# Performance work log

Hardware: AMD Instinct MI355X
Metric: run time of the kernel (lower is better)

The kernel has to match this reference:

```python
import jax, jax.numpy as jnp
import numpy as np
from jax import lax

# module config (matches init_kwargs)
IN_CHANNELS = 1
NUM_OR = 8               # 360 / angle_res(45)
THRESHOLD = 0.9
WINDOW = (5, 5)
STRIDE = (1, 1)
WINDOW_SCALE = float(WINDOW[0] * WINDOW[1])
NORMALIZE_COUNT = True   # normalize_count=True -> avg counts (avg_pool2d semantics)


def setup_inputs() -> dict:
    key = jax.random.key(0)
    k1, k2 = jax.random.split(key)
    x = jax.random.normal(k1, (16, IN_CHANNELS, 1024, 1024), dtype=jnp.float32)
    # edge-orientation masks (Sobel rotations in the original; values are fixed
    # buffers, so random stand-ins preserve the exact compute pattern)
    masks = jax.random.normal(k2, (IN_CHANNELS * NUM_OR, 1, 3, 3), dtype=jnp.float32)
    return {"x": x, "masks": masks}


def reference(x, masks):
    # grouped edge-filter conv: [B,C,H,W] x [C*O,1,3,3] -> [B,C*O,H-2,W-2]
    y = lax.conv_general_dilated(
        x, masks, window_strides=(1, 1), padding='VALID',
        rhs_dilation=(1, 1), feature_group_count=IN_CHANNELS,
        dimension_numbers=('NCHW', 'OIHW', 'NCHW'))
    value = jnp.max(y, axis=1)    # [B,H',W']
    index = jnp.argmax(y, axis=1)  # dominant orientation per pixel
    # below-threshold responses assigned to the extra 'no edge' bin
    index = jnp.where(value < THRESHOLD, NUM_OR, index)
    # one-hot over NUM_OR+1 bins -> [B, NUM_OR+1, H', W']
    bins = (index[:, None, :, :] ==
            jnp.arange(NUM_OR + 1)[None, :, None, None]).astype(jnp.float32)
    # windowed histogram counts (avg_pool2d with no padding => plain window mean)
    counts = lax.reduce_window(bins, 0.0, lax.add,
                               (1, 1) + WINDOW, (1, 1) + STRIDE, 'VALID')
    feat = counts / WINDOW_SCALE if NORMALIZE_COUNT else counts
    return feat  # [B, NUM_OR+1, H'-4, W'-4]
```

## Files before the change

### kernel.cpp

```cpp
#include <hip/hip_runtime.h>


#define BN   16
#define HH   1024
#define WW   1024
#define NOR  8
#define H2   1018
#define W2   1018
#define TH   16
#define TW   64
#define XH   (TH+6)
#define XW   (TW+6)
#define XWP  71
#define OHH  (TH+4)
#define OHW  (TW+4)
#define OHWP 69

__global__ __launch_bounds__(256)
void ehd_kernel(const float* __restrict__ x,
                const float* __restrict__ masks,
                float* __restrict__ out)
{
    __shared__ float xs[XH][XWP];
    __shared__ unsigned long long oh[OHH][OHWP];
    __shared__ unsigned long long rs[OHH][TW];

    const int tid = threadIdx.x;
    const int w0  = blockIdx.x * TW;
    const int h0  = blockIdx.y * TH;
    const int b   = blockIdx.z;

    float m[NOR][9];
#pragma unroll
    for (int o = 0; o < NOR; ++o)
#pragma unroll
        for (int t = 0; t < 9; ++t)
            m[o][t] = masks[o * 9 + t];

    const float* xb = x + (long)b * HH * WW;
    for (int t = tid; t < XH * XW; t += 256) {
        int i = t / XW, j = t - i * XW;
        int gh = h0 + i; if (gh > HH - 1) gh = HH - 1;
        int gw = w0 + j; if (gw > WW - 1) gw = WW - 1;
        xs[i][j] = xb[gh * WW + gw];
    }
    __syncthreads();

    for (int t = tid; t < OHH * OHW; t += 256) {
        int i = t / OHW, j = t - i * OHW;
        float xv[9];
#pragma unroll
        for (int di = 0; di < 3; ++di)
#pragma unroll
            for (int dj = 0; dj < 3; ++dj)
                xv[di * 3 + dj] = xs[i + di][j + dj];

        float best = 0.0f; int bi = 0;
#pragma unroll
        for (int o = 0; o < NOR; ++o) {
            float acc = xv[0] * m[o][0];
#pragma unroll
            for (int k = 1; k < 9; ++k)
                acc = fmaf(xv[k], m[o][k], acc);
            if (o == 0)          { best = acc; bi = 0; }
            else if (acc > best) { best = acc; bi = o; }
        }
        if (best < 0.9f) bi = NOR;
        oh[i][j] = 1ull << (7 * bi);
    }
    __syncthreads();

    for (int t = tid; t < OHH * TW; t += 256) {
        int i = t / TW, j = t - i * TW;
        unsigned long long s = oh[i][j];
#pragma unroll
        for (int d = 1; d < 5; ++d) s += oh[i][j + d];
        rs[i][j] = s;
    }
    __syncthreads();

    const int j  = tid & 63;
    const int i0 = tid >> 6;
    const int gw = w0 + j;
    for (int ii = i0; ii < TH; ii += 4) {
        const int gh = h0 + ii;
        unsigned long long s = rs[ii][j];
#pragma unroll
        for (int d = 1; d < 5; ++d) s += rs[ii + d][j];
        if (gh < H2 && gw < W2) {
#pragma unroll
            for (int k = 0; k < 9; ++k) {
                float c = (float)((unsigned)(s >> (7 * k)) & 0x7Fu);
                out[(((long)b * 9 + k) * H2 + gh) * W2 + gw] = c * (1.0f / 25.0f);
            }
        }
    }
}

extern "C" void kernel_launch(void* const* d_in, const int* in_sizes, int n_in,
                              void* d_out, int out_size, void* d_ws, size_t ws_size,
                              hipStream_t stream)
{
    const float* x     = (const float*)d_in[0];
    const float* masks = (const float*)d_in[1];
    float* out         = (float*)d_out;

    dim3 grid((W2 + TW - 1) / TW,
              (H2 + TH - 1) / TH,
              BN);
    ehd_kernel<<<grid, 256, 0, stream>>>(x, masks, out);
}
```

Baseline: 744.2 us.

## Switch to full-row blocks with rolling register window and ring-buffered row sums

Each block now handles 8 output rows across the full 1024-pixel width. It streams input rows through a 3-row register window with one row prefetched, and keeps a 5-slot ring of horizontal one-hot sums in shared memory. This replaces the 2D tiles whose halos recomputed conv/argmax on overlapping rows and columns, and it makes the output stores fully row-contiguous. In exchange, vertical halo recompute grows from 4 of 16 rows to 4 of 8, each row needs two block-wide barriers, and shared memory rises to about 48KB per block, which limits occupancy.

```diff
diff --git a/kernel.cpp b/kernel.cpp
--- a/kernel.cpp
+++ b/kernel.cpp
@@ -1,99 +1,125 @@
 #include <hip/hip_runtime.h>
 
 
-#define BN   16
-#define HH   1024
-#define WW   1024
-#define NOR  8
-#define H2   1018
-#define W2   1018
-#define TH   16
-#define TW   64
-#define XH   (TH+6)
-#define XW   (TW+6)
-#define XWP  71
-#define OHH  (TH+4)
-#define OHW  (TW+4)
-#define OHWP 69
+#define NOR 8
+#define HH  1024
+#define WW  1024
+#define H2  1018
+#define W2  1018
+#define RPB 8
+#define NIT (RPB + 4)
 
-__global__ __launch_bounds__(256)
-void ehd_kernel(const float* __restrict__ x,
-                const float* __restrict__ masks,
-                float* __restrict__ out)
+__global__ __launch_bounds__(256, 3)
+void ehd_rows(const float* __restrict__ x,
+              const float* __restrict__ masks,
+              float* __restrict__ out)
 {
-    __shared__ float xs[XH][XWP];
-    __shared__ unsigned long long oh[OHH][OHWP];
-    __shared__ unsigned long long rs[OHH][TW];
+    __shared__ unsigned long long ohrow[WW];
+    __shared__ unsigned long long rs[5][WW];
 
-    const int tid = threadIdx.x;
-    const int w0  = blockIdx.x * TW;
-    const int h0  = blockIdx.y * TH;
-    const int b   = blockIdx.z;
+    const int t  = threadIdx.x;
+    const int r0 = blockIdx.x * RPB;
+    const int b  = blockIdx.y;
+    const float* xb = x + (long)b * HH * WW;
 
     float m[NOR][9];
 #pragma unroll
     for (int o = 0; o < NOR; ++o)
 #pragma unroll
-        for (int t = 0; t < 9; ++t)
-            m[o][t] = masks[o * 9 + t];
+        for (int k = 0; k < 9; ++k)
+            m[o][k] = masks[o * 9 + k];
 
-    const float* xb = x + (long)b * HH * WW;
-    for (int t = tid; t < XH * XW; t += 256) {
-        int i = t / XW, j = t - i * XW;
-        int gh = h0 + i; if (gh > HH - 1) gh = HH - 1;
-        int gw = w0 + j; if (gw > WW - 1) gw = WW - 1;
-        xs[i][j] = xb[gh * WW + gw];
-    }
-    __syncthreads();
-
-    for (int t = tid; t < OHH * OHW; t += 256) {
-        int i = t / OHW, j = t - i * OHW;
-        float xv[9];
+    float wr[3][4][3];
 #pragma unroll
-        for (int di = 0; di < 3; ++di)
+    for (int s = 0; s < 3; ++s)
 #pragma unroll
-            for (int dj = 0; dj < 3; ++dj)
-                xv[di * 3 + dj] = xs[i + di][j + dj];
-
-        float best = 0.0f; int bi = 0;
+        for (int c = 0; c < 4; ++c) {
+            const int j = t + 256 * c;
 #pragma unroll
-        for (int o = 0; o < NOR; ++o) {
-            float acc = xv[0] * m[o][0];
-#pragma unroll
-            for (int k = 1; k < 9; ++k)
-                acc = fmaf(xv[k], m[o][k], acc);
-            if (o == 0)          { best = acc; bi = 0; }
-            else if (acc > best) { best = acc; bi = o; }
-        }
-        if (best < 0.9f) bi = NOR;
-        oh[i][j] = 1ull << (7 * bi);
-    }
-    __syncthreads();
-
-    for (int t = tid; t < OHH * TW; t += 256) {
-        int i = t / TW, j = t - i * TW;
-        unsigned long long s = oh[i][j];
-#pragma unroll
-        for (int d = 1; d < 5; ++d) s += oh[i][j + d];
-        rs[i][j] = s;
-    }
-    __syncthreads();
-
-    const int j  = tid & 63;
-    const int i0 = tid >> 6;
-    const int gw = w0 + j;
-    for (int ii = i0; ii < TH; ii += 4) {
-        const int gh = h0 + ii;
-        unsigned long long s = rs[ii][j];
-#pragma unroll
-        for (int d = 1; d < 5; ++d) s += rs[ii + d][j];
-        if (gh < H2 && gw < W2) {
-#pragma unroll
-            for (int k = 0; k < 9; ++k) {
-                float c = (float)((unsigned)(s >> (7 * k)) & 0x7Fu);
-                out[(((long)b * 9 + k) * H2 + gh) * W2 + gw] = c * (1.0f / 25.0f);
+            for (int d = 0; d < 3; ++d) {
+                int jj = j + d; if (jj > WW - 1) jj = WW - 1;
+                wr[s][c][d] = xb[(r0 + s) * WW + jj];
             }
         }
+
+    int slot = 0;
+    for (int rr = 0; rr < NIT; ++rr) {
+        float pf[4][3];
+        {
+            int nr = r0 + rr + 3; if (nr > HH - 1) nr = HH - 1;
+#pragma unroll
+            for (int c = 0; c < 4; ++c) {
+                const int j = t + 256 * c;
+#pragma unroll
+                for (int d = 0; d < 3; ++d) {
+                    int jj = j + d; if (jj > WW - 1) jj = WW - 1;
+                    pf[c][d] = xb[nr * WW + jj];
+                }
+            }
+        }
+
+#pragma unroll
+        for (int c = 0; c < 4; ++c) {
+            const int j = t + 256 * c;
+            if (j <= WW - 3) {
+                const float xv[9] = { wr[0][c][0], wr[0][c][1], wr[0][c][2],
+                                      wr[1][c][0], wr[1][c][1], wr[1][c][2],
+                                      wr[2][c][0], wr[2][c][1], wr[2][c][2] };
+                float best = 0.0f; int bi = 0;
+#pragma unroll
+                for (int o = 0; o < NOR; ++o) {
+                    float acc = xv[0] * m[o][0];
+#pragma unroll
+                    for (int k = 1; k < 9; ++k)
+                        acc = fmaf(xv[k], m[o][k], acc);
+                    if (o == 0)          { best = acc; bi = 0; }
+                    else if (acc > best) { best = acc; bi = o; }
+                }
+                if (best < 0.9f) bi = NOR;
+                ohrow[j] = 1ull << (7 * bi);
+            }
+        }
+        __syncthreads();
+
+#pragma unroll
+        for (int c = 0; c < 4; ++c) {
+            const int j = t + 256 * c;
+            if (j <= W2 - 1) {
+                unsigned long long s = ohrow[j] + ohrow[j + 1] + ohrow[j + 2]
+                                     + ohrow[j + 3] + ohrow[j + 4];
+                rs[slot][j] = s;
+            }
+        }
+
+        if (rr >= 4) {
+            const int ro = r0 + rr - 4;
+            if (ro < H2) {
+#pragma unroll
+                for (int c = 0; c < 4; ++c) {
+                    const int j = t + 256 * c;
+                    if (j <= W2 - 1) {
+                        unsigned long long s = rs[0][j] + rs[1][j] + rs[2][j]
+                                             + rs[3][j] + rs[4][j];
+#pragma unroll
+                        for (int k = 0; k < 9; ++k) {
+                            float cv = (float)((unsigned)(s >> (7 * k)) & 0x7Fu) * (1.0f / 25.0f);
+                            out[(((long)b * 9 + k) * H2 + ro) * W2 + j] = cv;
+                        }
+                    }
+                }
+            }
+        }
+        __syncthreads();
+
+#pragma unroll
+        for (int c = 0; c < 4; ++c)
+#pragma unroll
+            for (int d = 0; d < 3; ++d) {
+                wr[0][c][d] = wr[1][c][d];
+                wr[1][c][d] = wr[2][c][d];
+                wr[2][c][d] = pf[c][d];
+            }
+        slot = (slot == 4) ? 0 : slot + 1;
     }
 }
 
@@ -105,8 +131,7 @@
     const float* masks = (const float*)d_in[1];
     float* out         = (float*)d_out;
 
-    dim3 grid((W2 + TW - 1) / TW,
-              (H2 + TH - 1) / TH,
-              BN);
-    ehd_kernel<<<grid, 256, 0, stream>>>(x, masks, out);
+    dim3 grid((H2 + RPB - 1) / RPB,
+              16);
+    ehd_rows<<<grid, 256, 0, stream>>>(x, masks, out);
 }
```

After: 697.0 us. 6.3% less time.

## Replace shared-memory tiling with per-wavefront rolling-row stencil and shuffles

Applied to the files above, without the earlier changes.

Each wavefront now handles a 60-column strip over 16 output rows. It slides a 3-row register window down the rows, reading input directly from global memory with no LDS staging. The horizontal 5-wide window sum is done with lane shuffles, and the vertical sum with a 5-entry rolling register array, which removes the LDS tiles and all block barriers. In exchange, halo columns are recomputed per wavefront (4 of 64 lanes are overlap), and a fifth of the blocks' wavefronts exit immediately because 17 chunks don't divide by 4.

```diff
diff --git a/kernel.cpp b/kernel.cpp
--- a/kernel.cpp
+++ b/kernel.cpp
@@ -1,98 +1,100 @@
 #include <hip/hip_runtime.h>
 
 
-#define BN   16
-#define HH   1024
-#define WW   1024
-#define NOR  8
-#define H2   1018
-#define W2   1018
-#define TH   16
-#define TW   64
-#define XH   (TH+6)
-#define XW   (TW+6)
-#define XWP  71
-#define OHH  (TH+4)
-#define OHW  (TW+4)
-#define OHWP 69
+#define NOR 8
+#define HH  1024
+#define WW  1024
+#define H2  1018
+#define W2  1018
+#define RPW 16
+#define CW  60
+#define NCH 17
+#define PL  (H2 * W2)
 
-__global__ __launch_bounds__(256)
-void ehd_kernel(const float* __restrict__ x,
-                const float* __restrict__ masks,
-                float* __restrict__ out)
+__global__ __launch_bounds__(256, 4)
+void ehd_wave(const float* __restrict__ x,
+              const float* __restrict__ masks,
+              float* __restrict__ out)
 {
-    __shared__ float xs[XH][XWP];
-    __shared__ unsigned long long oh[OHH][OHWP];
-    __shared__ unsigned long long rs[OHH][TW];
+    const int lane  = threadIdx.x & 63;
+    const int wid   = threadIdx.x >> 6;
+    const int chunk = blockIdx.x * 4 + wid;
+    if (chunk >= NCH) return;
 
-    const int tid = threadIdx.x;
-    const int w0  = blockIdx.x * TW;
-    const int h0  = blockIdx.y * TH;
-    const int b   = blockIdx.z;
+    const int c0 = chunk * CW;
+    const int r0 = blockIdx.y * RPW;
+    const int b  = blockIdx.z;
+
+    const float* __restrict__ xb = x + (long)b * (HH * WW);
+    float* __restrict__ outb     = out + (long)b * 9 * PL;
 
     float m[NOR][9];
 #pragma unroll
     for (int o = 0; o < NOR; ++o)
 #pragma unroll
-        for (int t = 0; t < 9; ++t)
-            m[o][t] = masks[o * 9 + t];
+        for (int k = 0; k < 9; ++k)
+            m[o][k] = masks[o * 9 + k];
 
-    const float* xb = x + (long)b * HH * WW;
-    for (int t = tid; t < XH * XW; t += 256) {
-        int i = t / XW, j = t - i * XW;
-        int gh = h0 + i; if (gh > HH - 1) gh = HH - 1;
-        int gw = w0 + j; if (gw > WW - 1) gw = WW - 1;
-        xs[i][j] = xb[gh * WW + gw];
+    const int j  = c0 + lane;
+    const int ja = j     < 1023 ? j     : 1023;
+    const int jb = j + 1 < 1023 ? j + 1 : 1023;
+    const int jc = j + 2 < 1023 ? j + 2 : 1023;
+
+    float t00, t01, t02, t10, t11, t12;
+    {
+        const float* r = xb + r0 * WW;
+        t00 = r[ja]; t01 = r[jb]; t02 = r[jc];
+        r += WW;
+        t10 = r[ja]; t11 = r[jb]; t12 = r[jc];
     }
-    __syncthreads();
 
-    for (int t = tid; t < OHH * OHW; t += 256) {
-        int i = t / OHW, j = t - i * OHW;
-        float xv[9];
+    unsigned long long rs[5];
+
+    for (int g = 0; g < 4; ++g) {
 #pragma unroll
-        for (int di = 0; di < 3; ++di)
+        for (int p = 0; p < 5; ++p) {
+            const int it = g * 5 + p;
+
+            int hr = r0 + it + 2; if (hr > HH - 1) hr = HH - 1;
+            const float* rp = xb + hr * WW;
+            const float n0 = rp[ja], n1 = rp[jb], n2 = rp[jc];
+
+            const float xv[9] = { t00, t01, t02, t10, t11, t12, n0, n1, n2 };
+            float best = 0.0f; int bi = 0;
 #pragma unroll
-            for (int dj = 0; dj < 3; ++dj)
-                xv[di * 3 + dj] = xs[i + di][j + dj];
+            for (int o = 0; o < NOR; ++o) {
+                float acc = xv[0] * m[o][0];
+#pragma unroll
+                for (int k = 1; k < 9; ++k)
+                    acc = fmaf(xv[k], m[o][k], acc);
+                if (o == 0)          { best = acc; bi = 0; }
+                else if (acc > best) { best = acc; bi = o; }
+            }
+            if (best < 0.9f) bi = NOR;
 
-        float best = 0.0f; int bi = 0;
+            const int b1 = __shfl(bi, lane + 1);
+            const int b2 = __shfl(bi, lane + 2);
+            const int b3 = __shfl(bi, lane + 3);
+            const int b4 = __shfl(bi, lane + 4);
+            rs[p] = (1ull << (7 * bi)) + (1ull << (7 * b1)) + (1ull << (7 * b2))
+                  + (1ull << (7 * b3)) + (1ull << (7 * b4));
+
+            if (it >= 4) {
+                const int ro = r0 + it - 4;
+                if (ro < H2 && lane < CW && j < W2) {
+                    const unsigned long long s = rs[0] + rs[1] + rs[2] + rs[3] + rs[4];
+                    const unsigned off0 = (unsigned)ro * W2 + (unsigned)j;
 #pragma unroll
-        for (int o = 0; o < NOR; ++o) {
-            float acc = xv[0] * m[o][0];
-#pragma unroll
-            for (int k = 1; k < 9; ++k)
-                acc = fmaf(xv[k], m[o][k], acc);
-            if (o == 0)          { best = acc; bi = 0; }
-            else if (acc > best) { best = acc; bi = o; }
-        }
-        if (best < 0.9f) bi = NOR;
-        oh[i][j] = 1ull << (7 * bi);
-    }
-    __syncthreads();
+                    for (int k = 0; k < 9; ++k) {
+                        const float cv =
+                            (float)((unsigned)(s >> (7 * k)) & 0x7Fu) * (1.0f / 25.0f);
+                        outb[off0 + (unsigned)(k * PL)] = cv;
+                    }
+                }
+            }
 
-    for (int t = tid; t < OHH * TW; t += 256) {
-        int i = t / TW, j = t - i * TW;
-        unsigned long long s = oh[i][j];
-#pragma unroll
-        for (int d = 1; d < 5; ++d) s += oh[i][j + d];
-        rs[i][j] = s;
-    }
-    __syncthreads();
-
-    const int j  = tid & 63;
-    const int i0 = tid >> 6;
-    const int gw = w0 + j;
-    for (int ii = i0; ii < TH; ii += 4) {
-        const int gh = h0 + ii;
-        unsigned long long s = rs[ii][j];
-#pragma unroll
-        for (int d = 1; d < 5; ++d) s += rs[ii + d][j];
-        if (gh < H2 && gw < W2) {
-#pragma unroll
-            for (int k = 0; k < 9; ++k) {
-                float c = (float)((unsigned)(s >> (7 * k)) & 0x7Fu);
-                out[(((long)b * 9 + k) * H2 + gh) * W2 + gw] = c * (1.0f / 25.0f);
-            }
+            t00 = t10; t01 = t11; t02 = t12;
+            t10 = n0;  t11 = n1;  t12 = n2;
         }
     }
 }
@@ -105,8 +107,8 @@
     const float* masks = (const float*)d_in[1];
     float* out         = (float*)d_out;
 
-    dim3 grid((W2 + TW - 1) / TW,
-              (H2 + TH - 1) / TH,
-              BN);
-    ehd_kernel<<<grid, 256, 0, stream>>>(x, masks, out);
+    dim3 grid((NCH + 3) / 4,
+              (H2 + RPW - 1) / RPW,
+              16);
+    ehd_wave<<<grid, 256, 0, stream>>>(x, masks, out);
 }
```

Result: no change. 743.3 us (-0.1%).
